# Performance work log

Hardware: AMD Instinct MI355X
Metric: run time of the kernel (lower is better)

## Reference

```python
import jax, jax.numpy as jnp
import numpy as np

B, T_SUB, L, H, K = 64, 512, 256, 1024, 9


def setup_inputs() -> dict:
    key = jax.random.key(0)
    ks = jax.random.split(key, 8)
    sequence_output = jax.random.normal(ks[0], (B, T_SUB, H), jnp.float32)
    attention_mask = jnp.ones((B, T_SUB), jnp.int32)
    offsets = jnp.sort(jax.random.randint(ks[1], (B, L), 0, T_SUB), axis=1)
    mask = jnp.ones((B, L), bool)
    labels = jax.random.randint(ks[2], (B, L), 0, K)
    classifier_w = jax.random.normal(ks[3], (H, K), jnp.float32) / np.sqrt(H).astype(np.float32)
    classifier_b = jnp.zeros((K,), jnp.float32)
    start_transitions = jax.random.uniform(ks[4], (K,), jnp.float32, -0.1, 0.1)
    end_transitions = jax.random.uniform(ks[5], (K,), jnp.float32, -0.1, 0.1)
    transitions = jax.random.uniform(ks[6], (K, K), jnp.float32, -0.1, 0.1)
    return {
        'sequence_output': sequence_output, 'attention_mask': attention_mask,
        'offsets': offsets, 'mask': mask, 'labels': labels,
        'classifier_w': classifier_w, 'classifier_b': classifier_b,
        'start_transitions': start_transitions, 'end_transitions': end_transitions,
        'transitions': transitions,
    }


def crf_log_likelihood(emissions, tags, mask_b, start, trans, end):
    # emissions [B,L,K], tags [B,L] int, mask_b [B,L] bool (mask[:,0] all True)
    maskf = mask_b.astype(emissions.dtype)
    # numerator: score of the gold path
    first_tag = tags[:, 0]
    score = start[first_tag] + jnp.take_along_axis(emissions[:, 0], first_tag[:, None], 1)[:, 0]
    trans_sc = trans[tags[:, :-1], tags[:, 1:]]                                   # [B,L-1]
    emit_sc = jnp.take_along_axis(emissions[:, 1:], tags[:, 1:, None], 2)[..., 0]  # [B,L-1]
    score = score + jnp.sum((trans_sc + emit_sc) * maskf[:, 1:], axis=1)
    seq_ends = jnp.sum(mask_b.astype(jnp.int32), axis=1) - 1
    last_tags = jnp.take_along_axis(tags, seq_ends[:, None], 1)[:, 0]
    score = score + end[last_tags]
    # denominator: log partition via scan over time
    def step(alpha, xs):
        em_i, m_i = xs  # [B,K], [B]
        nxt = jax.nn.logsumexp(alpha[:, :, None] + trans[None] + em_i[:, None, :], axis=1)
        return jnp.where(m_i[:, None], nxt, alpha), None
    alpha0 = start[None] + emissions[:, 0]
    xs = (jnp.swapaxes(emissions[:, 1:], 0, 1), jnp.swapaxes(mask_b[:, 1:], 0, 1))
    alphaL, _ = jax.lax.scan(step, alpha0, xs)
    denom = jax.nn.logsumexp(alphaL + end[None], axis=1)
    return score - denom


def crf_viterbi(emissions, mask_b, start, trans, end):
    k = emissions.shape[-1]
    iden = jnp.arange(k)[None, :]
    def step(score, xs):
        em_i, m_i = xs
        cand = score[:, :, None] + trans[None]     # [B,K_prev,K_cur]
        idx = jnp.argmax(cand, axis=1)             # [B,K]
        nxt = jnp.max(cand, axis=1) + em_i
        score = jnp.where(m_i[:, None], nxt, score)
        idx = jnp.where(m_i[:, None], idx, iden)   # identity through padding
        return score, idx
    score0 = start[None] + emissions[:, 0]
    xs = (jnp.swapaxes(emissions[:, 1:], 0, 1), jnp.swapaxes(mask_b[:, 1:], 0, 1))
    final, hist = jax.lax.scan(step, score0, xs)   # hist [L-1,B,K]
    last = jnp.argmax(final + end[None], axis=1)   # [B]
    def back(tag, h):
        prev = jnp.take_along_axis(h, tag[:, None], 1)[:, 0]
        return prev, tag
    tag0, ys = jax.lax.scan(back, last, hist, reverse=True)  # ys[i] = tag_{i+1}
    path = jnp.concatenate([tag0[None], ys], axis=0)          # [L,B]
    return jnp.swapaxes(path, 0, 1)


def reference(sequence_output, attention_mask, offsets, mask, labels,
              classifier_w, classifier_b, start_transitions, end_transitions, transitions):
    # embedder: sub_token_mode='first' -> gather first-subtoken embedding per word
    embed = jnp.take_along_axis(sequence_output, offsets[:, :, None], axis=1)  # [B,L,H]
    # dropout is identity at inference
    logits = embed @ classifier_w + classifier_b                               # [B,L,K]
    crf_mask = mask                                                            # word-level CRF mask
    tags = labels * crf_mask.astype(labels.dtype)
    llh = crf_log_likelihood(logits, tags, crf_mask, start_transitions, transitions, end_transitions)
    loss = -jnp.mean(llh)
    predicts = crf_viterbi(logits, crf_mask, start_transitions, transitions, end_transitions)
    predicts = predicts * crf_mask.astype(predicts.dtype)
    return loss, logits, predicts
```

## Files before the change

kernel.cpp:

```cpp
#include <hip/hip_runtime.h>
#include <hip/hip_bf16.h>
#include <math.h>

#define BB 64
#define TSUB 512
#define LL 256
#define HH 1024
#define KK 9

__device__ __forceinline__ float bcast(float v, int lane) {
    return __int_as_float(__builtin_amdgcn_readlane(__float_as_int(v), lane));
}

__global__ __launch_bounds__(256) void logits_kernel(
    const float* __restrict__ seq,
    const int*   __restrict__ offsets,
    const float* __restrict__ w,
    const float* __restrict__ bias,
    float*       __restrict__ logits)
{
    __shared__ float w_s[KK][HH];
    const int tid = threadIdx.x;

    for (int i = tid; i < HH * KK; i += 256) {
        int h = i / KK, k = i - h * KK;
        w_s[k][h] = w[i];
    }
    __syncthreads();

    const int wave = tid >> 6;
    const int lane = tid & 63;
    const int row0 = (blockIdx.x * 4 + wave) * 4;

    const float* src[4];
    float acc[4][KK];
#pragma unroll
    for (int r = 0; r < 4; ++r) {
        int row = row0 + r;
        int b = row >> 8;
        int l = row & 255;
        int off = offsets[b * LL + l];
        src[r] = seq + ((size_t)(b * TSUB + off)) * HH;
#pragma unroll
        for (int k = 0; k < KK; ++k) acc[r][k] = 0.0f;
    }

#pragma unroll
    for (int c = 0; c < 4; ++c) {
        const int h0 = c * 256 + lane * 4;
        float4 x[4];
#pragma unroll
        for (int r = 0; r < 4; ++r) x[r] = *(const float4*)(src[r] + h0);
#pragma unroll
        for (int k = 0; k < KK; ++k) {
            float4 wv = *(const float4*)&w_s[k][h0];
#pragma unroll
            for (int r = 0; r < 4; ++r) {
                acc[r][k] += x[r].x * wv.x + x[r].y * wv.y +
                             x[r].z * wv.z + x[r].w * wv.w;
            }
        }
    }

#pragma unroll
    for (int r = 0; r < 4; ++r) {
#pragma unroll
        for (int k = 0; k < KK; ++k) {
            float v = acc[r][k];
#pragma unroll
            for (int d = 32; d; d >>= 1) v += __shfl_xor(v, d, 64);
            acc[r][k] = v;
        }
    }

    if (lane == 0) {
#pragma unroll
        for (int r = 0; r < 4; ++r) {
#pragma unroll
            for (int k = 0; k < KK; ++k) {
                logits[(size_t)(row0 + r) * KK + k] = acc[r][k] + bias[k];
            }
        }
    }
}

__global__ __launch_bounds__(256) void crf_kernel(
    const float* __restrict__ logits,
    const int*   __restrict__ labels,
    const float* __restrict__ start_t,
    const float* __restrict__ end_t,
    const float* __restrict__ trans,
    float*       __restrict__ predicts,
    float*       __restrict__ llh_ws)
{
    __shared__ float em[LL * KK];
    __shared__ int   lab[LL];
    __shared__ int   hist[(LL - 1) * KK];
    __shared__ int   path[LL];
    __shared__ float s_start[KK], s_end[KK], s_trans[KK * KK];
    __shared__ float s_denom, s_score;

    const int b = blockIdx.x;
    const int tid = threadIdx.x;

    for (int i = tid; i < LL * KK; i += 256)
        em[i] = logits[(size_t)b * LL * KK + i];
    for (int i = tid; i < LL; i += 256)
        lab[i] = labels[b * LL + i];
    if (tid < KK) { s_start[tid] = start_t[tid]; s_end[tid] = end_t[tid]; }
    if (tid < KK * KK) s_trans[tid] = trans[tid];
    __syncthreads();

    const int wave = tid >> 6;
    const int lane = tid & 63;
    const int j = (lane < KK) ? lane : 0;

    if (wave == 0) {
        float tcol[KK];
#pragma unroll
        for (int i = 0; i < KK; ++i) tcol[i] = s_trans[i * KK + j];

        float a = s_start[j] + em[j];
        float emv = em[KK + j];
        for (int t = 1; t < LL; ++t) {
            float em_cur = emv;
            if (t + 1 < LL) emv = em[(t + 1) * KK + j];
            float cand[KK];
#pragma unroll
            for (int i = 0; i < KK; ++i) cand[i] = bcast(a, i) + tcol[i];
            float m = fmaxf(fmaxf(fmaxf(cand[0], cand[1]), cand[2]),
                     fmaxf(fmaxf(fmaxf(cand[3], cand[4]), cand[5]),
                           fmaxf(fmaxf(cand[6], cand[7]), cand[8])));
            float sum = 0.0f;
#pragma unroll
            for (int i = 0; i < KK; ++i) sum += __expf(cand[i] - m);
            a = m + __logf(sum) + em_cur;
        }
        float v = a + s_end[j];
        float c[KK];
#pragma unroll
        for (int i = 0; i < KK; ++i) c[i] = bcast(v, i);
        float m = c[0];
#pragma unroll
        for (int i = 1; i < KK; ++i) m = fmaxf(m, c[i]);
        float sum = 0.0f;
#pragma unroll
        for (int i = 0; i < KK; ++i) sum += __expf(c[i] - m);
        if (lane == 0) s_denom = m + __logf(sum);
    } else if (wave == 1) {
        float tcol[KK];
#pragma unroll
        for (int i = 0; i < KK; ++i) tcol[i] = s_trans[i * KK + j];

        float vs = s_start[j] + em[j];
        float emv = em[KK + j];
        for (int t = 1; t < LL; ++t) {
            float em_cur = emv;
            if (t + 1 < LL) emv = em[(t + 1) * KK + j];
            float cand[KK];
#pragma unroll
            for (int i = 0; i < KK; ++i) cand[i] = bcast(vs, i) + tcol[i];
            float m = fmaxf(fmaxf(fmaxf(cand[0], cand[1]), cand[2]),
                     fmaxf(fmaxf(fmaxf(cand[3], cand[4]), cand[5]),
                           fmaxf(fmaxf(cand[6], cand[7]), cand[8])));
            vs = m + em_cur;
            int bi = KK - 1;
#pragma unroll
            for (int i = KK - 2; i >= 0; --i) bi = (cand[i] == m) ? i : bi;
            if (lane < KK) hist[(t - 1) * KK + j] = bi;
        }
        float v = vs + s_end[j];
        float c[KK];
#pragma unroll
        for (int i = 0; i < KK; ++i) c[i] = bcast(v, i);
        float bv = c[0];
        int bj = 0;
#pragma unroll
        for (int i = 1; i < KK; ++i) { if (c[i] > bv) { bv = c[i]; bj = i; } }
        if (lane == 0) {
            int cur = bj;
            path[LL - 1] = cur;
            for (int t = LL - 2; t >= 0; --t) {
                cur = hist[t * KK + cur];
                path[t] = cur;
            }
        }
    } else if (wave == 2) {
        float part = 0.0f;
        for (int t = 1 + lane; t < LL; t += 64) {
            int tp = lab[t - 1], tc = lab[t];
            part += s_trans[tp * KK + tc] + em[t * KK + tc];
        }
#pragma unroll
        for (int d = 32; d; d >>= 1) part += __shfl_xor(part, d, 64);
        if (lane == 0) {
            int t0 = lab[0], tl = lab[LL - 1];
            s_score = part + s_start[t0] + em[t0] + s_end[tl];
        }
    }
    __syncthreads();

    for (int i = tid; i < LL; i += 256)
        predicts[b * LL + i] = (float)path[i];
    if (tid == 0) llh_ws[b] = s_score - s_denom;
}

__global__ void loss_kernel(const float* __restrict__ llh_ws,
                            float* __restrict__ out)
{
    const int lane = threadIdx.x;
    float v = llh_ws[lane];
#pragma unroll
    for (int d = 32; d; d >>= 1) v += __shfl_xor(v, d, 64);
    if (lane == 0) out[0] = -v / (float)BB;
}

extern "C" void kernel_launch(void* const* d_in, const int* in_sizes, int n_in,
                              void* d_out, int out_size, void* d_ws, size_t ws_size,
                              hipStream_t stream)
{
    (void)in_sizes; (void)n_in; (void)out_size; (void)ws_size;

    const float* seq     = (const float*)d_in[0];
    const int*   offsets = (const int*)d_in[2];
    const int*   labels  = (const int*)d_in[4];
    const float* w       = (const float*)d_in[5];
    const float* bias    = (const float*)d_in[6];
    const float* start_t = (const float*)d_in[7];
    const float* end_t   = (const float*)d_in[8];
    const float* trans   = (const float*)d_in[9];

    float* out      = (float*)d_out;
    float* logits   = out + 1;
    float* predicts = out + 1 + BB * LL * KK;
    float* llh_ws   = (float*)d_ws;

    logits_kernel<<<(BB * LL) / 16, 256, 0, stream>>>(seq, offsets, w, bias, logits);
    crf_kernel<<<BB, 256, 0, stream>>>(logits, labels, start_t, end_t, trans,
                                       predicts, llh_ws);
    loss_kernel<<<1, 64, 0, stream>>>(llh_ws, out);
}
```

Measured before the change: 263.1 us.

## Restructure logits mapping, base-2 shifted logsumexp, and chunked parallel Viterbi backtrace

The logits kernel now gives each row to four lanes instead of a whole wave. That raises rows per block to 64 and replaces the full-wave shuffle reduction with a two-step one. The forward CRF recursion now works in base 2 with hardware exp2/log2 and takes lane 0's alpha as the reference, which removes the 9-way max and one exp per step. The Viterbi backtrace is split into 7 chunks whose boundary maps are built in parallel, then resolved serially and expanded in parallel. Using lane 0 instead of the true max as the reference risks overflow in exp2 when scores diverge widely.

```diff
diff --git a/kernel.cpp b/kernel.cpp
--- a/kernel.cpp
+++ b/kernel.cpp
@@ -8,9 +8,14 @@
 #define HH 1024
 #define KK 9
 
+#define S_CHUNK 37
+#define N_CHUNK 7
+
 __device__ __forceinline__ float bcast(float v, int lane) {
     return __int_as_float(__builtin_amdgcn_readlane(__float_as_int(v), lane));
 }
+__device__ __forceinline__ float fexp2(float x) { return __builtin_amdgcn_exp2f(x); }
+__device__ __forceinline__ float flog2(float x) { return __builtin_amdgcn_logf(x); }
 
 __global__ __launch_bounds__(256) void logits_kernel(
     const float* __restrict__ seq,
@@ -30,57 +35,42 @@
 
     const int wave = tid >> 6;
     const int lane = tid & 63;
-    const int row0 = (blockIdx.x * 4 + wave) * 4;
-
-    const float* src[4];
-    float acc[4][KK];
-#pragma unroll
-    for (int r = 0; r < 4; ++r) {
-        int row = row0 + r;
-        int b = row >> 8;
-        int l = row & 255;
-        int off = offsets[b * LL + l];
-        src[r] = seq + ((size_t)(b * TSUB + off)) * HH;
-#pragma unroll
-        for (int k = 0; k < KK; ++k) acc[r][k] = 0.0f;
-    }
-
-#pragma unroll
-    for (int c = 0; c < 4; ++c) {
-        const int h0 = c * 256 + lane * 4;
-        float4 x[4];
-#pragma unroll
-        for (int r = 0; r < 4; ++r) x[r] = *(const float4*)(src[r] + h0);
+    const int r_local = lane >> 2;
+    const int s = lane & 3;
+
+    const int row = blockIdx.x * 64 + wave * 16 + r_local;
+    const int b = row >> 8;
+    const int l = row & 255;
+    const int off = offsets[b * LL + l];
+    const float* __restrict__ src = seq + ((size_t)(b * TSUB + off)) * HH;
+
+    float acc[KK];
+#pragma unroll
+    for (int k = 0; k < KK; ++k) acc[k] = 0.0f;
+
+#pragma unroll 4
+    for (int i = 0; i < 64; ++i) {
+        const int h0 = i * 16 + s * 4;
+        float4 x = *(const float4*)(src + h0);
 #pragma unroll
         for (int k = 0; k < KK; ++k) {
             float4 wv = *(const float4*)&w_s[k][h0];
-#pragma unroll
-            for (int r = 0; r < 4; ++r) {
-                acc[r][k] += x[r].x * wv.x + x[r].y * wv.y +
-                             x[r].z * wv.z + x[r].w * wv.w;
-            }
-        }
-    }
-
-#pragma unroll
-    for (int r = 0; r < 4; ++r) {
-#pragma unroll
-        for (int k = 0; k < KK; ++k) {
-            float v = acc[r][k];
-#pragma unroll
-            for (int d = 32; d; d >>= 1) v += __shfl_xor(v, d, 64);
-            acc[r][k] = v;
-        }
-    }
-
-    if (lane == 0) {
-#pragma unroll
-        for (int r = 0; r < 4; ++r) {
-#pragma unroll
-            for (int k = 0; k < KK; ++k) {
-                logits[(size_t)(row0 + r) * KK + k] = acc[r][k] + bias[k];
-            }
-        }
+            acc[k] += x.x * wv.x + x.y * wv.y + x.z * wv.z + x.w * wv.w;
+        }
+    }
+
+#pragma unroll
+    for (int k = 0; k < KK; ++k) {
+        float v = acc[k];
+        v += __shfl_xor(v, 1, 64);
+        v += __shfl_xor(v, 2, 64);
+        acc[k] = v;
+    }
+
+    if (s == 0) {
+#pragma unroll
+        for (int k = 0; k < KK; ++k)
+            logits[(size_t)row * KK + k] = acc[k] + bias[k];
     }
 }
 
@@ -93,21 +83,26 @@
     float*       __restrict__ predicts,
     float*       __restrict__ llh_ws)
 {
-    __shared__ float em[LL * KK];
+    __shared__ float em2[LL * KK];
     __shared__ int   lab[LL];
     __shared__ int   hist[(LL - 1) * KK];
     __shared__ int   path[LL];
-    __shared__ float s_start[KK], s_end[KK], s_trans[KK * KK];
+    __shared__ float s_trans[KK * KK];
+    __shared__ int   Fmap[N_CHUNK * KK];
+    __shared__ int   s_bnd[N_CHUNK + 1];
     __shared__ float s_denom, s_score;
+
+    const float LOG2E = 1.4426950408889634f;
+    const float LN2   = 0.6931471805599453f;
 
     const int b = blockIdx.x;
     const int tid = threadIdx.x;
+    const float* __restrict__ base = logits + (size_t)b * LL * KK;
 
     for (int i = tid; i < LL * KK; i += 256)
-        em[i] = logits[(size_t)b * LL * KK + i];
+        em2[i] = base[i] * LOG2E;
     for (int i = tid; i < LL; i += 256)
         lab[i] = labels[b * LL + i];
-    if (tid < KK) { s_start[tid] = start_t[tid]; s_end[tid] = end_t[tid]; }
     if (tid < KK * KK) s_trans[tid] = trans[tid];
     __syncthreads();
 
@@ -116,27 +111,31 @@
     const int j = (lane < KK) ? lane : 0;
 
     if (wave == 0) {
-        float tcol[KK];
-#pragma unroll
-        for (int i = 0; i < KK; ++i) tcol[i] = s_trans[i * KK + j];
-
-        float a = s_start[j] + em[j];
-        float emv = em[KK + j];
+        float tcol2[KK], dt2[KK];
+#pragma unroll
+        for (int i = 0; i < KK; ++i) tcol2[i] = trans[i * KK + j] * LOG2E;
+#pragma unroll
+        for (int i = 1; i < KK; ++i) dt2[i] = tcol2[i] - tcol2[0];
+        const float endj2 = end_t[j] * LOG2E;
+
+        float a2 = start_t[j] * LOG2E + em2[j];
+        float emv = em2[KK + j];
         for (int t = 1; t < LL; ++t) {
             float em_cur = emv;
-            if (t + 1 < LL) emv = em[(t + 1) * KK + j];
-            float cand[KK];
-#pragma unroll
-            for (int i = 0; i < KK; ++i) cand[i] = bcast(a, i) + tcol[i];
-            float m = fmaxf(fmaxf(fmaxf(cand[0], cand[1]), cand[2]),
-                     fmaxf(fmaxf(fmaxf(cand[3], cand[4]), cand[5]),
-                           fmaxf(fmaxf(cand[6], cand[7]), cand[8])));
-            float sum = 0.0f;
-#pragma unroll
-            for (int i = 0; i < KK; ++i) sum += __expf(cand[i] - m);
-            a = m + __logf(sum) + em_cur;
-        }
-        float v = a + s_end[j];
+            if (t + 1 < LL) emv = em2[(t + 1) * KK + j];
+            float sa0 = bcast(a2, 0);
+            float d = a2 - sa0;
+            float q[KK];
+#pragma unroll
+            for (int i = 1; i < KK; ++i) q[i] = bcast(d, i) + dt2[i];
+            float e1 = fexp2(q[1]), e2 = fexp2(q[2]);
+            float e3 = fexp2(q[3]), e4 = fexp2(q[4]);
+            float e5 = fexp2(q[5]), e6 = fexp2(q[6]);
+            float e7 = fexp2(q[7]), e8 = fexp2(q[8]);
+            float sum = (((e1 + e2) + (e3 + e4)) + ((e5 + e6) + (e7 + e8))) + 1.0f;
+            a2 = sa0 + tcol2[0] + flog2(sum) + em_cur;
+        }
+        float v = a2 + endj2;
         float c[KK];
 #pragma unroll
         for (int i = 0; i < KK; ++i) c[i] = bcast(v, i);
@@ -145,21 +144,22 @@
         for (int i = 1; i < KK; ++i) m = fmaxf(m, c[i]);
         float sum = 0.0f;
 #pragma unroll
-        for (int i = 0; i < KK; ++i) sum += __expf(c[i] - m);
-        if (lane == 0) s_denom = m + __logf(sum);
+        for (int i = 0; i < KK; ++i) sum += fexp2(c[i] - m);
+        if (lane == 0) s_denom = (m + flog2(sum)) * LN2;
     } else if (wave == 1) {
-        float tcol[KK];
-#pragma unroll
-        for (int i = 0; i < KK; ++i) tcol[i] = s_trans[i * KK + j];
-
-        float vs = s_start[j] + em[j];
-        float emv = em[KK + j];
+        float tcol2[KK];
+#pragma unroll
+        for (int i = 0; i < KK; ++i) tcol2[i] = trans[i * KK + j] * LOG2E;
+        const float endj2 = end_t[j] * LOG2E;
+
+        float vs = start_t[j] * LOG2E + em2[j];
+        float emv = em2[KK + j];
         for (int t = 1; t < LL; ++t) {
             float em_cur = emv;
-            if (t + 1 < LL) emv = em[(t + 1) * KK + j];
+            if (t + 1 < LL) emv = em2[(t + 1) * KK + j];
             float cand[KK];
 #pragma unroll
-            for (int i = 0; i < KK; ++i) cand[i] = bcast(vs, i) + tcol[i];
+            for (int i = 0; i < KK; ++i) cand[i] = bcast(vs, i) + tcol2[i];
             float m = fmaxf(fmaxf(fmaxf(cand[0], cand[1]), cand[2]),
                      fmaxf(fmaxf(fmaxf(cand[3], cand[4]), cand[5]),
                            fmaxf(fmaxf(cand[6], cand[7]), cand[8])));
@@ -167,35 +167,59 @@
             int bi = KK - 1;
 #pragma unroll
             for (int i = KK - 2; i >= 0; --i) bi = (cand[i] == m) ? i : bi;
-            if (lane < KK) hist[(t - 1) * KK + j] = bi;
-        }
-        float v = vs + s_end[j];
+            hist[(t - 1) * KK + j] = bi;
+        }
+        float v = vs + endj2;
         float c[KK];
 #pragma unroll
         for (int i = 0; i < KK; ++i) c[i] = bcast(v, i);
         float bv = c[0];
-        int bj = 0;
-#pragma unroll
-        for (int i = 1; i < KK; ++i) { if (c[i] > bv) { bv = c[i]; bj = i; } }
+        int last = 0;
+#pragma unroll
+        for (int i = 1; i < KK; ++i) { if (c[i] > bv) { bv = c[i]; last = i; } }
+
+        if (lane < N_CHUNK * KK) {
+            const int cid = lane / KK;
+            const int jj  = lane - cid * KK;
+            const int lo = cid * S_CHUNK;
+            int hi = lo + S_CHUNK;
+            if (hi > LL - 1) hi = LL - 1;
+            hi -= 1;
+            int f = jj;
+            for (int r = hi; r >= lo; --r) f = hist[r * KK + f];
+            Fmap[cid * KK + jj] = f;
+        }
         if (lane == 0) {
-            int cur = bj;
-            path[LL - 1] = cur;
-            for (int t = LL - 2; t >= 0; --t) {
-                cur = hist[t * KK + cur];
-                path[t] = cur;
+            s_bnd[N_CHUNK] = last;
+            int st = last;
+            for (int c2 = N_CHUNK - 1; c2 >= 0; --c2) {
+                st = Fmap[c2 * KK + st];
+                s_bnd[c2] = st;
             }
         }
+        if (lane < N_CHUNK) {
+            const int lo = lane * S_CHUNK;
+            int hi = lo + S_CHUNK;
+            if (hi > LL - 1) hi = LL - 1;
+            hi -= 1;
+            int x = s_bnd[lane + 1];
+            for (int r = hi; r >= lo; --r) {
+                x = hist[r * KK + x];
+                path[r] = x;
+            }
+        }
+        if (lane == 0) path[LL - 1] = last;
     } else if (wave == 2) {
         float part = 0.0f;
         for (int t = 1 + lane; t < LL; t += 64) {
             int tp = lab[t - 1], tc = lab[t];
-            part += s_trans[tp * KK + tc] + em[t * KK + tc];
+            part += s_trans[tp * KK + tc] + base[t * KK + tc];
         }
 #pragma unroll
         for (int d = 32; d; d >>= 1) part += __shfl_xor(part, d, 64);
         if (lane == 0) {
             int t0 = lab[0], tl = lab[LL - 1];
-            s_score = part + s_start[t0] + em[t0] + s_end[tl];
+            s_score = part + start_t[t0] + base[t0] + end_t[tl];
         }
     }
     __syncthreads();
@@ -235,7 +259,7 @@
     float* predicts = out + 1 + BB * LL * KK;
     float* llh_ws   = (float*)d_ws;
 
-    logits_kernel<<<(BB * LL) / 16, 256, 0, stream>>>(seq, offsets, w, bias, logits);
+    logits_kernel<<<(BB * LL) / 64, 256, 0, stream>>>(seq, offsets, w, bias, logits);
     crf_kernel<<<BB, 256, 0, stream>>>(logits, labels, start_t, end_t, trans,
                                        predicts, llh_ws);
     loss_kernel<<<1, 64, 0, stream>>>(llh_ws, out);
```

Measured after the change: 260.0 us. No clear change (-1.2%).
